# Kernel optimization log

Hardware: AMD Instinct MI355X
Metric: run time of the kernel (lower is better)

The kernel has to match this reference:

```python
import jax, jax.numpy as jnp
import numpy as np

EMBED_DIM = 1024
NUM_HEADS = 16
HEAD_DIM = EMBED_DIM // NUM_HEADS
B, S = 2, 2048


def setup_inputs() -> dict:
    key = jax.random.key(0)
    ks = jax.random.split(key, 12)
    sd = 1.0 / np.sqrt(EMBED_DIM)
    def lin(kw, kb):
        W = jax.random.uniform(kw, (EMBED_DIM, EMBED_DIM), jnp.float32, -sd, sd)
        b = jax.random.uniform(kb, (EMBED_DIM,), jnp.float32, -sd, sd)
        return W, b
    Wq, bq = lin(ks[0], ks[1])
    Wk, bk = lin(ks[2], ks[3])
    Wv, bv = lin(ks[4], ks[5])
    Wo, bo = lin(ks[6], ks[7])
    q = jax.random.normal(ks[8], (B, S, EMBED_DIM), jnp.float32)
    k = jax.random.normal(ks[9], (B, S, EMBED_DIM), jnp.float32)
    v = jax.random.normal(ks[10], (B, S, EMBED_DIM), jnp.float32)
    # broadcastable causal mask: True = keep (mask==0 positions get -inf)
    attn_mask = jnp.tril(jnp.ones((S, S), jnp.bool_))[None, None]
    return {"q": q, "k": k, "v": v,
            "Wq": Wq, "bq": bq, "Wk": Wk, "bk": bk,
            "Wv": Wv, "bv": bv, "Wo": Wo, "bo": bo,
            "attn_mask": attn_mask}


def reference(q, k, v, Wq, bq, Wk, bk, Wv, bv, Wo, bo, attn_mask):
    bsz, tgt_len, _ = q.shape
    src_len = k.shape[1]
    scale = jnp.sqrt(jnp.float32(HEAD_DIM))
    # projections: PyTorch Linear is x @ W.T + b
    qh = (q @ Wq.T + bq).reshape(bsz, tgt_len, NUM_HEADS, HEAD_DIM).transpose(0, 2, 1, 3)
    kh = (k @ Wk.T + bk).reshape(bsz, src_len, NUM_HEADS, HEAD_DIM).transpose(0, 2, 1, 3)
    vh = (v @ Wv.T + bv).reshape(bsz, src_len, NUM_HEADS, HEAD_DIM).transpose(0, 2, 1, 3)
    # [B,H,T,S] scores
    scores = jnp.einsum('bhtd,bhsd->bhts', qh, kh) / scale
    scores = jnp.where(attn_mask, scores, -jnp.inf)
    attn = jax.nn.softmax(scores, axis=-1)
    out = jnp.einsum('bhts,bhsd->bhtd', attn, vh)  # [B,H,T,D]
    out = out.transpose(0, 2, 1, 3).reshape(bsz, tgt_len, EMBED_DIM)
    return out @ Wo.T + bo
```

## Files before the change

### kernel.cpp

```cpp
#include <hip/hip_runtime.h>
#include <hip/hip_bf16.h>
#include <stdint.h>
#include <stddef.h>

typedef __hip_bfloat16 bf16_t;
typedef __attribute__((ext_vector_type(8))) short short8;
typedef __attribute__((ext_vector_type(4))) short short4v;
typedef __attribute__((ext_vector_type(4))) float floatx4;

#define EMBED 1024
#define NHEAD 16
#define HDIM  64
#define BATCH 2
#define SEQ   2048
#define MTOT  (BATCH*SEQ)
#define NEG_INF (-1e30f)
#define SCALE2 0.18033688011112042f

#define MFMA16(a,b,c) __builtin_amdgcn_mfma_f32_16x16x32_bf16(a,b,c,0,0,0)

static __device__ __forceinline__ short bf16_bits(float x) {
    return __builtin_bit_cast(short, __float2bfloat16(x));
}

static __device__ __forceinline__ float fast_exp2(float x) {
#if __has_builtin(__builtin_amdgcn_exp2f)
    return __builtin_amdgcn_exp2f(x);
#else
    return __expf(x * 0.6931471805599453f);
#endif
}

static __device__ __forceinline__ void async_ld16(const bf16_t* g, short* l) {
    __builtin_amdgcn_global_load_lds(
        (const __attribute__((address_space(1))) void*)g,
        (__attribute__((address_space(3))) void*)l,
        16, 0, 0);
}

static __device__ __forceinline__ void store_out(float* p, float v)  { *p = v; }
static __device__ __forceinline__ void store_out(bf16_t* p, float v) { *p = __float2bfloat16(v); }

__global__ __launch_bounds__(256)
void cvt_all(const float* __restrict__ q, const float* __restrict__ k, const float* __restrict__ v,
             const float* __restrict__ wq, const float* __restrict__ wk,
             const float* __restrict__ wv, const float* __restrict__ wo,
             bf16_t* __restrict__ Qx, bf16_t* __restrict__ Kx, bf16_t* __restrict__ Vx,
             bf16_t* __restrict__ Wqb, bf16_t* __restrict__ Wkb,
             bf16_t* __restrict__ Wvb, bf16_t* __restrict__ Wob)
{
    const float* s; bf16_t* d; int n;
    switch (blockIdx.y) {
        case 0:  s = q;  d = Qx;  n = MTOT * EMBED;  break;
        case 1:  s = k;  d = Kx;  n = MTOT * EMBED;  break;
        case 2:  s = v;  d = Vx;  n = MTOT * EMBED;  break;
        case 3:  s = wq; d = Wqb; n = EMBED * EMBED; break;
        case 4:  s = wk; d = Wkb; n = EMBED * EMBED; break;
        case 5:  s = wv; d = Wvb; n = EMBED * EMBED; break;
        default: s = wo; d = Wob; n = EMBED * EMBED; break;
    }
    const int i4 = (int)blockIdx.x * 256 + (int)threadIdx.x;
    if (i4 * 4 < n) {
        const float4 f = ((const float4*)s)[i4];
        short4v o;
        o[0] = bf16_bits(f.x); o[1] = bf16_bits(f.y);
        o[2] = bf16_bits(f.z); o[3] = bf16_bits(f.w);
        ((short4v*)d)[i4] = o;
    }
}

template <typename OutT, bool VT>
static __device__ __forceinline__ void gemm_tile_128(
    const bf16_t* __restrict__ A, const bf16_t* __restrict__ W,
    const float* __restrict__ bias, OutT* __restrict__ C)
{
    const int N = 1024, K = 1024;
    __shared__ alignas(16) short As[128*32];
    __shared__ alignas(16) short Bs[128*32];

    const int tid  = threadIdx.x;
    const int wave = tid >> 6;
    const int lane = tid & 63;
    const int nbn = N >> 7;
    const int bm = (int)blockIdx.x / nbn;
    const int bn = (int)blockIdx.x % nbn;
    const int m0 = bm << 7, n0 = bn << 7;

    const int wm = ((wave >> 1) & 1) << 6;
    const int wn = (wave & 1) << 6;

    floatx4 acc[4][4] = {};

    const int srow = (wave << 5) + (lane >> 2);
    const int scol = (lane & 3) << 3;
    const bf16_t* gA = A + (size_t)(m0 + srow) * K + scol;
    const bf16_t* gB = W + (size_t)(n0 + srow) * K + scol;
    short* lA0 = &As[(wave << 10)];
    short* lA1 = &As[(wave << 10) + 512];
    short* lB0 = &Bs[(wave << 10)];
    short* lB1 = &Bs[(wave << 10) + 512];

    const int fr = lane & 15;
    const int fk = (lane >> 4) << 3;

    for (int k0 = 0; k0 < K; k0 += 32) {
        __syncthreads();
        async_ld16(gA,                  lA0);
        async_ld16(gA + (size_t)16 * K, lA1);
        async_ld16(gB,                  lB0);
        async_ld16(gB + (size_t)16 * K, lB1);
        gA += 32; gB += 32;
        __syncthreads();

        short8 af[4], bfr[4];
        #pragma unroll
        for (int i = 0; i < 4; ++i)
            af[i] = *(const short8*)&As[(wm + (i << 4) + fr) * 32 + fk];
        #pragma unroll
        for (int j = 0; j < 4; ++j)
            bfr[j] = *(const short8*)&Bs[(wn + (j << 4) + fr) * 32 + fk];
        #pragma unroll
        for (int i = 0; i < 4; ++i)
            #pragma unroll
            for (int j = 0; j < 4; ++j)
                acc[i][j] = MFMA16(af[i], bfr[j], acc[i][j]);
    }

    const int q4 = (lane >> 4) << 2;
    #pragma unroll
    for (int j = 0; j < 4; ++j) {
        const int n = n0 + wn + (j << 4) + fr;
        const float bv = bias[n];
        #pragma unroll
        for (int i = 0; i < 4; ++i) {
            const int mb = m0 + wm + (i << 4) + q4;
            if (VT) {
                const int bb = mb >> 11, ss = mb & 2047;
                short4v pk;
                #pragma unroll
                for (int r = 0; r < 4; ++r)
                    pk[r] = bf16_bits(acc[i][j][r] + bv);
                *(short4v*)((bf16_t*)C + ((size_t)(bb * 1024 + n) << 11) + ss) = pk;
            } else {
                #pragma unroll
                for (int r = 0; r < 4; ++r)
                    store_out(&C[(size_t)(mb + r) * N + n], acc[i][j][r] + bv);
            }
        }
    }
}

__global__ __launch_bounds__(256)
void qkv_proj(const bf16_t* __restrict__ xq, const bf16_t* __restrict__ xk,
              const bf16_t* __restrict__ xv,
              const bf16_t* __restrict__ Wq, const bf16_t* __restrict__ Wk,
              const bf16_t* __restrict__ Wv,
              const float* __restrict__ bq, const float* __restrict__ bk,
              const float* __restrict__ bv,
              bf16_t* __restrict__ Qp, bf16_t* __restrict__ Kp, bf16_t* __restrict__ Vtp)
{
    if (blockIdx.z == 0)      gemm_tile_128<bf16_t, false>(xq, Wq, bq, Qp);
    else if (blockIdx.z == 1) gemm_tile_128<bf16_t, false>(xk, Wk, bk, Kp);
    else                      gemm_tile_128<bf16_t, true >(xv, Wv, bv, Vtp);
}

__global__ __launch_bounds__(256)
void out_proj(const bf16_t* __restrict__ AO, const bf16_t* __restrict__ Wo,
              const float* __restrict__ bo, float* __restrict__ out)
{
    gemm_tile_128<float, false>(AO, Wo, bo, out);
}

__global__ __launch_bounds__(64)
void attn_causal(const bf16_t* __restrict__ Qp, const bf16_t* __restrict__ Kp,
                 const bf16_t* __restrict__ Vt, bf16_t* __restrict__ AO)
{
    __shared__ alignas(16) short Pbuf[2][16 * 40];

    const int lane = (int)threadIdx.x & 63;
    const int bid  = (int)blockIdx.x;
    const int bh   = bid & 31;
    const int tile = 63 - (bid >> 5);
    const int b = bh >> 4, h = bh & 15;
    const int q0  = tile << 5;
    const int nch = tile + 1;

    const int fr   = lane & 15;
    const int quad = lane >> 4;
    const int fk   = quad << 3;

    const bf16_t* Q0 = Qp + (size_t)(b * SEQ + q0 + fr) * EMBED + h * HDIM;
    const short8 aq00 = *(const short8*)(Q0 + fk);
    const short8 aq01 = *(const short8*)(Q0 + 32 + fk);
    const short8 aq10 = *(const short8*)(Q0 + (size_t)16 * EMBED + fk);
    const short8 aq11 = *(const short8*)(Q0 + (size_t)16 * EMBED + 32 + fk);

    const bf16_t* Kbase = Kp + (size_t)(b * SEQ) * EMBED + h * HDIM;
    const bf16_t* Vbase = Vt + ((size_t)(b * 1024 + h * HDIM) << 11);

    floatx4 o0[4] = {}, o1[4] = {};
    float m0 = NEG_INF, m1 = NEG_INF;
    float l0 = 0.f, l1 = 0.f;

    short* Pw0 = &Pbuf[0][0];
    short* Pw1 = &Pbuf[1][0];

    auto smax = [&](const floatx4& sA, const floatx4& sB, float& m_u, float& l_u,
                    floatx4* o_u, short* PwU, const bool diag, const int u16) -> short8 {
        float v0[4], v1[4];
        float mx = NEG_INF;
        #pragma unroll
        for (int r = 0; r < 4; ++r) {
            float a  = sA[r] * SCALE2;
            float bb = sB[r] * SCALE2;
            if (diag) {
                const int kq = (quad << 2) + r;
                const int lq = u16 + fr;
                if (kq > lq)      a  = NEG_INF;
                if (kq + 16 > lq) bb = NEG_INF;
            }
            v0[r] = a; v1[r] = bb;
            mx = fmaxf(mx, fmaxf(a, bb));
        }
        mx = fmaxf(mx, __shfl_xor(mx, 16, 64));
        mx = fmaxf(mx, __shfl_xor(mx, 32, 64));
        const float mo = m_u;
        const bool need = __any(mx > mo + 8.0f) != 0;
        const float mn = need ? fmaxf(mo, mx) : mo;
        float ls = 0.f;
        #pragma unroll
        for (int r = 0; r < 4; ++r) {
            v0[r] = fast_exp2(v0[r] - mn);
            v1[r] = fast_exp2(v1[r] - mn);
            ls += v0[r] + v1[r];
        }
        ls += __shfl_xor(ls, 16, 64);
        ls += __shfl_xor(ls, 32, 64);
        if (need) {
            const float al = fast_exp2(mo - mn);
            m_u = mn;
            l_u = l_u * al + ls;
            #pragma unroll
            for (int r = 0; r < 4; ++r) {
                const float ao = __shfl(al, (lane & 48) | ((quad << 2) + r), 64);
                #pragma unroll
                for (int t = 0; t < 4; ++t) o_u[t][r] *= ao;
            }
        } else {
            l_u += ls;
        }
        short4v w0, w1;
        #pragma unroll
        for (int r = 0; r < 4; ++r) { w0[r] = bf16_bits(v0[r]); w1[r] = bf16_bits(v1[r]); }
        *(short4v*)&PwU[fr * 40 + (quad << 2)]      = w0;
        *(short4v*)&PwU[fr * 40 + 16 + (quad << 2)] = w1;
        __asm__ volatile("" ::: "memory");
        const short8 pa = *(const short8*)&PwU[fr * 40 + fk];
        __asm__ volatile("" ::: "memory");
        return pa;
    };

#define KLOAD(K0_, K1_, K2_, K3_, kvo) do {                                  \
        const bf16_t* Kr0_ = Kbase + (size_t)((kvo) + fr) * EMBED;           \
        const bf16_t* Kr1_ = Kr0_ + (size_t)16 * EMBED;                      \
        K0_ = *(const short8*)(Kr0_ + fk);                                   \
        K1_ = *(const short8*)(Kr0_ + 32 + fk);                              \
        K2_ = *(const short8*)(Kr1_ + fk);                                   \
        K3_ = *(const short8*)(Kr1_ + 32 + fk);                              \
    } while (0)

#define ITER(KC0, KC1, KC2, KC3, KN0, KN1, KN2, KN3, DIAGF) do {             \
        const int kv0 = c << 5;                                              \
           \
        const short8 vf0 = *(const short8*)(Vbase + ((size_t)(fr)      << 11) + kv0 + fk); \
        const short8 vf1 = *(const short8*)(Vbase + ((size_t)(16 + fr) << 11) + kv0 + fk); \
        const short8 vf2 = *(const short8*)(Vbase + ((size_t)(32 + fr) << 11) + kv0 + fk); \
        const short8 vf3 = *(const short8*)(Vbase + ((size_t)(48 + fr) << 11) + kv0 + fk); \
        floatx4 s00 = {}, s01 = {}, s10 = {}, s11 = {};                      \
        s00 = MFMA16(KC0, aq00, s00); s00 = MFMA16(KC1, aq01, s00);          \
        s10 = MFMA16(KC0, aq10, s10); s10 = MFMA16(KC1, aq11, s10);          \
        s01 = MFMA16(KC2, aq00, s01); s01 = MFMA16(KC3, aq01, s01);          \
        s11 = MFMA16(KC2, aq10, s11); s11 = MFMA16(KC3, aq11, s11);          \
        if (c + 1 < nch) { KLOAD(KN0, KN1, KN2, KN3, kv0 + 32); }            \
        const short8 pa0 = smax(s00, s01, m0, l0, o0, Pw0, DIAGF, 0);        \
        const short8 pa1 = smax(s10, s11, m1, l1, o1, Pw1, DIAGF, 16);       \
        o0[0] = MFMA16(pa0, vf0, o0[0]); o1[0] = MFMA16(pa1, vf0, o1[0]);    \
        o0[1] = MFMA16(pa0, vf1, o0[1]); o1[1] = MFMA16(pa1, vf1, o1[1]);    \
        o0[2] = MFMA16(pa0, vf2, o0[2]); o1[2] = MFMA16(pa1, vf2, o1[2]);    \
        o0[3] = MFMA16(pa0, vf3, o0[3]); o1[3] = MFMA16(pa1, vf3, o1[3]);    \
    } while (0)

    short8 ka0, ka1, ka2, ka3, kb0, kb1, kb2, kb3;
    KLOAD(ka0, ka1, ka2, ka3, 0);

    int c = 0;
    if (nch > 1) {
        for (;;) {
            ITER(ka0, ka1, ka2, ka3, kb0, kb1, kb2, kb3, false);
            if (++c == nch - 1) break;
            ITER(kb0, kb1, kb2, kb3, ka0, ka1, ka2, ka3, false);
            if (++c == nch - 1) break;
        }
    }
    if (c & 1) { ITER(kb0, kb1, kb2, kb3, ka0, ka1, ka2, ka3, true); }
    else       { ITER(ka0, ka1, ka2, ka3, kb0, kb1, kb2, kb3, true); }

#undef ITER
#undef KLOAD

    const float r0 = 1.0f / l0;
    const float r1 = 1.0f / l1;
    #pragma unroll
    for (int r = 0; r < 4; ++r) {
        const int src = (lane & 48) | ((quad << 2) + r);
        const float i0 = __shfl(r0, src, 64);
        const float i1 = __shfl(r1, src, 64);
        const int row0 = q0 + (quad << 2) + r;
        bf16_t* out0 = AO + (size_t)(b * SEQ + row0) * EMBED + h * HDIM + fr;
        bf16_t* out1 = out0 + (size_t)16 * EMBED;
        #pragma unroll
        for (int t = 0; t < 4; ++t) {
            out0[t << 4] = __float2bfloat16(o0[t][r] * i0);
            out1[t << 4] = __float2bfloat16(o1[t][r] * i1);
        }
    }
}

extern "C" void kernel_launch(void* const* d_in, const int* in_sizes, int n_in,
                              void* d_out, int out_size, void* d_ws, size_t ws_size,
                              hipStream_t stream)
{
    (void)in_sizes; (void)n_in; (void)out_size; (void)ws_size;
    const float* q  = (const float*)d_in[0];
    const float* k  = (const float*)d_in[1];
    const float* v  = (const float*)d_in[2];
    const float* Wq = (const float*)d_in[3];
    const float* bq = (const float*)d_in[4];
    const float* Wk = (const float*)d_in[5];
    const float* bk = (const float*)d_in[6];
    const float* Wv = (const float*)d_in[7];
    const float* bv = (const float*)d_in[8];
    const float* Wo = (const float*)d_in[9];
    const float* bo = (const float*)d_in[10];

    const size_t NX = (size_t)MTOT * EMBED;
    const size_t NW = (size_t)EMBED * EMBED;
    bf16_t* Qx  = (bf16_t*)d_ws;
    bf16_t* Kx  = Qx  + NX;
    bf16_t* Vx  = Kx  + NX;
    bf16_t* Wqb = Vx  + NX;
    bf16_t* Wkb = Wqb + NW;
    bf16_t* Wvb = Wkb + NW;
    bf16_t* Wob = Wvb + NW;
    bf16_t* Qp  = Wob + NW;
    bf16_t* Kp  = Qp  + NX;
    bf16_t* Vtp = Kp  + NX;
    bf16_t* AO  = Vtp + NX;

    dim3 blk(256);
    cvt_all<<<dim3(4096, 7), blk, 0, stream>>>(q, k, v, Wq, Wk, Wv, Wo,
                                               Qx, Kx, Vx, Wqb, Wkb, Wvb, Wob);
    qkv_proj<<<dim3(256, 1, 3), blk, 0, stream>>>(Qx, Kx, Vx, Wqb, Wkb, Wvb,
                                                  bq, bk, bv, Qp, Kp, Vtp);
    attn_causal<<<dim3(2048), dim3(64), 0, stream>>>(Qp, Kp, Vtp, AO);
    out_proj<<<dim3(256), blk, 0, stream>>>(AO, Wob, bo, (float*)d_out);
}
```

Measured before the change: 284.8 us.

## Split long causal attention tiles across two blocks and merge partials

The 32 longest query tiles per head are split into two halves of the key range, each run by its own block, which writes unnormalized fp32 partial outputs plus row max and row sum to workspace. A new combine kernel then merges the two halves with log-sum-exp weighting. The goal is to balance the causal triangle and shorten the critical path of the attention kernel. The softmax is also reworked to skip the cross-lane max and sum reductions unless a rescale is needed, deferring the row-sum reduction to the end. This costs an extra kernel launch and the workspace traffic for the partials.

```diff
diff --git a/kernel.cpp b/kernel.cpp
--- a/kernel.cpp
+++ b/kernel.cpp
@@ -173,17 +173,35 @@
 
 __global__ __launch_bounds__(64)
 void attn_causal(const bf16_t* __restrict__ Qp, const bf16_t* __restrict__ Kp,
-                 const bf16_t* __restrict__ Vt, bf16_t* __restrict__ AO)
+                 const bf16_t* __restrict__ Vt, bf16_t* __restrict__ AO,
+                 float* __restrict__ Op, float* __restrict__ Mp, float* __restrict__ Lp)
 {
     __shared__ alignas(16) short Pbuf[2][16 * 40];
 
     const int lane = (int)threadIdx.x & 63;
     const int bid  = (int)blockIdx.x;
     const int bh   = bid & 31;
-    const int tile = 63 - (bid >> 5);
+    const int w    = bid >> 5;
+    int tile, sidx, c0, c1;
+    bool split;
+    if (w < 64) {
+        tile  = 63 - (w >> 1);
+        sidx  = w & 1;
+        split = true;
+        const int nch = tile + 1;
+        const int h1  = (nch + 1) >> 1;
+        c0 = sidx ? h1 : 0;
+        c1 = sidx ? nch : h1;
+    } else {
+        tile  = 95 - w;
+        sidx  = 0;
+        split = false;
+        c0 = 0;
+        c1 = tile + 1;
+    }
+    const bool hasdiag = (c1 == tile + 1);
     const int b = bh >> 4, h = bh & 15;
-    const int q0  = tile << 5;
-    const int nch = tile + 1;
+    const int q0 = tile << 5;
 
     const int fr   = lane & 15;
     const int quad = lane >> 4;
@@ -205,9 +223,9 @@
     short* Pw0 = &Pbuf[0][0];
     short* Pw1 = &Pbuf[1][0];
 
-    auto smax = [&](const floatx4& sA, const floatx4& sB, float& m_u, float& l_u,
-                    floatx4* o_u, short* PwU, const bool diag, const int u16) -> short8 {
-        float v0[4], v1[4];
+    auto smax_vals = [&](const floatx4& sA, const floatx4& sB, float& m_u, float& l_u,
+                         floatx4* o_u, const bool diag, const int u16,
+                         float* v0, float* v1) {
         float mx = NEG_INF;
         #pragma unroll
         for (int r = 0; r < 4; ++r) {
@@ -222,42 +240,28 @@
             v0[r] = a; v1[r] = bb;
             mx = fmaxf(mx, fmaxf(a, bb));
         }
-        mx = fmaxf(mx, __shfl_xor(mx, 16, 64));
-        mx = fmaxf(mx, __shfl_xor(mx, 32, 64));
-        const float mo = m_u;
-        const bool need = __any(mx > mo + 8.0f) != 0;
-        const float mn = need ? fmaxf(mo, mx) : mo;
-        float ls = 0.f;
-        #pragma unroll
-        for (int r = 0; r < 4; ++r) {
-            v0[r] = fast_exp2(v0[r] - mn);
-            v1[r] = fast_exp2(v1[r] - mn);
-            ls += v0[r] + v1[r];
-        }
-        ls += __shfl_xor(ls, 16, 64);
-        ls += __shfl_xor(ls, 32, 64);
-        if (need) {
-            const float al = fast_exp2(mo - mn);
+        if (__any(mx > m_u + 8.0f)) {
+            mx = fmaxf(mx, __shfl_xor(mx, 16, 64));
+            mx = fmaxf(mx, __shfl_xor(mx, 32, 64));
+            const float mn = fmaxf(m_u, mx);
+            const float al = fast_exp2(m_u - mn);
             m_u = mn;
-            l_u = l_u * al + ls;
+            l_u *= al;
             #pragma unroll
             for (int r = 0; r < 4; ++r) {
                 const float ao = __shfl(al, (lane & 48) | ((quad << 2) + r), 64);
                 #pragma unroll
                 for (int t = 0; t < 4; ++t) o_u[t][r] *= ao;
             }
-        } else {
-            l_u += ls;
-        }
-        short4v w0, w1;
-        #pragma unroll
-        for (int r = 0; r < 4; ++r) { w0[r] = bf16_bits(v0[r]); w1[r] = bf16_bits(v1[r]); }
-        *(short4v*)&PwU[fr * 40 + (quad << 2)]      = w0;
-        *(short4v*)&PwU[fr * 40 + 16 + (quad << 2)] = w1;
-        __asm__ volatile("" ::: "memory");
-        const short8 pa = *(const short8*)&PwU[fr * 40 + fk];
-        __asm__ volatile("" ::: "memory");
-        return pa;
+        }
+        float ls = 0.f;
+        #pragma unroll
+        for (int r = 0; r < 4; ++r) {
+            v0[r] = fast_exp2(v0[r] - m_u);
+            v1[r] = fast_exp2(v1[r] - m_u);
+            ls += v0[r] + v1[r];
+        }
+        l_u += ls;
     };
 
 #define KLOAD(K0_, K1_, K2_, K3_, kvo) do {                                  \
@@ -269,7 +273,7 @@
         K3_ = *(const short8*)(Kr1_ + 32 + fk);                              \
     } while (0)
 
-#define ITER(KC0, KC1, KC2, KC3, KN0, KN1, KN2, KN3, DIAGF) do {             \
+#define ITER(KC0, KC1, KC2, KC3, KN0, KN1, KN2, KN3, DIAGF, PREF) do {       \
         const int kv0 = c << 5;                                              \
            \
         const short8 vf0 = *(const short8*)(Vbase + ((size_t)(fr)      << 11) + kv0 + fk); \
@@ -281,9 +285,24 @@
         s10 = MFMA16(KC0, aq10, s10); s10 = MFMA16(KC1, aq11, s10);          \
         s01 = MFMA16(KC2, aq00, s01); s01 = MFMA16(KC3, aq01, s01);          \
         s11 = MFMA16(KC2, aq10, s11); s11 = MFMA16(KC3, aq11, s11);          \
-        if (c + 1 < nch) { KLOAD(KN0, KN1, KN2, KN3, kv0 + 32); }            \
-        const short8 pa0 = smax(s00, s01, m0, l0, o0, Pw0, DIAGF, 0);        \
-        const short8 pa1 = smax(s10, s11, m1, l1, o1, Pw1, DIAGF, 16);       \
+        if (PREF) { KLOAD(KN0, KN1, KN2, KN3, kv0 + 32); }                   \
+        float p00[4], p01[4], p10[4], p11[4];                                \
+        smax_vals(s00, s01, m0, l0, o0, DIAGF, 0,  p00, p01);                \
+        smax_vals(s10, s11, m1, l1, o1, DIAGF, 16, p10, p11);                \
+        short4v wa0, wa1, wb0, wb1;                                          \
+        _Pragma("unroll")                                                    \
+        for (int r = 0; r < 4; ++r) {                                        \
+            wa0[r] = bf16_bits(p00[r]); wa1[r] = bf16_bits(p01[r]);          \
+            wb0[r] = bf16_bits(p10[r]); wb1[r] = bf16_bits(p11[r]);          \
+        }                                                                    \
+        *(short4v*)&Pw0[fr * 40 + (quad << 2)]      = wa0;                   \
+        *(short4v*)&Pw0[fr * 40 + 16 + (quad << 2)] = wa1;                   \
+        *(short4v*)&Pw1[fr * 40 + (quad << 2)]      = wb0;                   \
+        *(short4v*)&Pw1[fr * 40 + 16 + (quad << 2)] = wb1;                   \
+        __asm__ volatile("" ::: "memory");     \
+        const short8 pa0 = *(const short8*)&Pw0[fr * 40 + fk];               \
+        const short8 pa1 = *(const short8*)&Pw1[fr * 40 + fk];               \
+        __asm__ volatile("" ::: "memory");                                   \
         o0[0] = MFMA16(pa0, vf0, o0[0]); o1[0] = MFMA16(pa1, vf0, o1[0]);    \
         o0[1] = MFMA16(pa0, vf1, o0[1]); o1[1] = MFMA16(pa1, vf1, o1[1]);    \
         o0[2] = MFMA16(pa0, vf2, o0[2]); o1[2] = MFMA16(pa1, vf2, o1[2]);    \
@@ -291,39 +310,103 @@
     } while (0)
 
     short8 ka0, ka1, ka2, ka3, kb0, kb1, kb2, kb3;
-    KLOAD(ka0, ka1, ka2, ka3, 0);
-
-    int c = 0;
-    if (nch > 1) {
+    KLOAD(ka0, ka1, ka2, ka3, c0 << 5);
+
+    int c = c0;
+    const int cl = c1 - 1;
+    if (cl > c0) {
         for (;;) {
-            ITER(ka0, ka1, ka2, ka3, kb0, kb1, kb2, kb3, false);
-            if (++c == nch - 1) break;
-            ITER(kb0, kb1, kb2, kb3, ka0, ka1, ka2, ka3, false);
-            if (++c == nch - 1) break;
-        }
-    }
-    if (c & 1) { ITER(kb0, kb1, kb2, kb3, ka0, ka1, ka2, ka3, true); }
-    else       { ITER(ka0, ka1, ka2, ka3, kb0, kb1, kb2, kb3, true); }
+            ITER(ka0, ka1, ka2, ka3, kb0, kb1, kb2, kb3, false, true);
+            if (++c == cl) break;
+            ITER(kb0, kb1, kb2, kb3, ka0, ka1, ka2, ka3, false, true);
+            if (++c == cl) break;
+        }
+    }
+    if ((c - c0) & 1) { ITER(kb0, kb1, kb2, kb3, ka0, ka1, ka2, ka3, hasdiag, false); }
+    else              { ITER(ka0, ka1, ka2, ka3, kb0, kb1, kb2, kb3, hasdiag, false); }
 
 #undef ITER
 #undef KLOAD
 
-    const float r0 = 1.0f / l0;
-    const float r1 = 1.0f / l1;
-    #pragma unroll
-    for (int r = 0; r < 4; ++r) {
-        const int src = (lane & 48) | ((quad << 2) + r);
-        const float i0 = __shfl(r0, src, 64);
-        const float i1 = __shfl(r1, src, 64);
-        const int row0 = q0 + (quad << 2) + r;
-        bf16_t* out0 = AO + (size_t)(b * SEQ + row0) * EMBED + h * HDIM + fr;
-        bf16_t* out1 = out0 + (size_t)16 * EMBED;
-        #pragma unroll
-        for (int t = 0; t < 4; ++t) {
-            out0[t << 4] = __float2bfloat16(o0[t][r] * i0);
-            out1[t << 4] = __float2bfloat16(o1[t][r] * i1);
-        }
-    }
+    { float t = __shfl_xor(l0, 16, 64); l0 += t; t = __shfl_xor(l0, 32, 64); l0 += t; }
+    { float t = __shfl_xor(l1, 16, 64); l1 += t; t = __shfl_xor(l1, 32, 64); l1 += t; }
+
+    if (!split) {
+        const float r0 = 1.0f / l0;
+        const float r1 = 1.0f / l1;
+        #pragma unroll
+        for (int r = 0; r < 4; ++r) {
+            const int src = (lane & 48) | ((quad << 2) + r);
+            const float i0 = __shfl(r0, src, 64);
+            const float i1 = __shfl(r1, src, 64);
+            const int row0 = q0 + (quad << 2) + r;
+            bf16_t* out0 = AO + (size_t)(b * SEQ + row0) * EMBED + h * HDIM + fr;
+            bf16_t* out1 = out0 + (size_t)16 * EMBED;
+            #pragma unroll
+            for (int t = 0; t < 4; ++t) {
+                out0[t << 4] = __float2bfloat16(o0[t][r] * i0);
+                out1[t << 4] = __float2bfloat16(o1[t][r] * i1);
+            }
+        }
+    } else {
+        const int p = (bh << 5) | (tile - 32);
+        float* Ob = Op + (((size_t)sidx << 10) + p) * 2048;
+        #pragma unroll
+        for (int r = 0; r < 4; ++r) {
+            const int row0 = (quad << 2) + r;
+            #pragma unroll
+            for (int t = 0; t < 4; ++t) {
+                Ob[row0 * 64 + (t << 4) + fr]        = o0[t][r];
+                Ob[(16 + row0) * 64 + (t << 4) + fr] = o1[t][r];
+            }
+        }
+        if (quad == 0) {
+            const size_t mb = (((size_t)sidx << 10) + p) * 32;
+            Mp[mb + fr]      = m0;
+            Mp[mb + 16 + fr] = m1;
+            Lp[mb + fr]      = l0;
+            Lp[mb + 16 + fr] = l1;
+        }
+    }
+}
+
+__global__ __launch_bounds__(256)
+void attn_combine(const float* __restrict__ Op, const float* __restrict__ Mp,
+                  const float* __restrict__ Lp, bf16_t* __restrict__ AO)
+{
+    const int p   = (int)blockIdx.x;
+    const int tid = (int)threadIdx.x;
+    const int row = tid >> 3;
+    const int d0  = (tid & 7) << 3;
+    const int bh = p >> 5, tile = 32 + (p & 31);
+    const int b = bh >> 4, h = bh & 15;
+
+    const float m0 = Mp[(size_t)p * 32 + row];
+    const float m1 = Mp[(size_t)(1024 + p) * 32 + row];
+    const float l0 = Lp[(size_t)p * 32 + row];
+    const float l1 = Lp[(size_t)(1024 + p) * 32 + row];
+    const float M  = fmaxf(m0, m1);
+    const float w0 = fast_exp2(m0 - M);
+    const float w1 = fast_exp2(m1 - M);
+    const float rd = 1.0f / (l0 * w0 + l1 * w1);
+
+    const float* O0 = Op + ((size_t)p << 11) + row * 64 + d0;
+    const float* O1 = O0 + ((size_t)1024 << 11);
+    const float4 a0 = *(const float4*)O0;
+    const float4 a1 = *(const float4*)(O0 + 4);
+    const float4 c0 = *(const float4*)O1;
+    const float4 c1 = *(const float4*)(O1 + 4);
+
+    short8 pk;
+    pk[0] = bf16_bits((a0.x * w0 + c0.x * w1) * rd);
+    pk[1] = bf16_bits((a0.y * w0 + c0.y * w1) * rd);
+    pk[2] = bf16_bits((a0.z * w0 + c0.z * w1) * rd);
+    pk[3] = bf16_bits((a0.w * w0 + c0.w * w1) * rd);
+    pk[4] = bf16_bits((a1.x * w0 + c1.x * w1) * rd);
+    pk[5] = bf16_bits((a1.y * w0 + c1.y * w1) * rd);
+    pk[6] = bf16_bits((a1.z * w0 + c1.z * w1) * rd);
+    pk[7] = bf16_bits((a1.w * w0 + c1.w * w1) * rd);
+    *(short8*)(AO + (size_t)(b * SEQ + tile * 32 + row) * EMBED + h * HDIM + d0) = pk;
 }
 
 extern "C" void kernel_launch(void* const* d_in, const int* in_sizes, int n_in,
@@ -357,11 +440,16 @@
     bf16_t* Vtp = Kp  + NX;
     bf16_t* AO  = Vtp + NX;
 
+    float* Op = (float*)Qx;
+    float* Mp = (float*)Wqb;
+    float* Lp = Mp + 2 * 1024 * 32;
+
     dim3 blk(256);
     cvt_all<<<dim3(4096, 7), blk, 0, stream>>>(q, k, v, Wq, Wk, Wv, Wo,
                                                Qx, Kx, Vx, Wqb, Wkb, Wvb, Wob);
     qkv_proj<<<dim3(256, 1, 3), blk, 0, stream>>>(Qx, Kx, Vx, Wqb, Wkb, Wvb,
                                                   bq, bk, bv, Qp, Kp, Vtp);
-    attn_causal<<<dim3(2048), dim3(64), 0, stream>>>(Qp, Kp, Vtp, AO);
+    attn_causal<<<dim3(3072), dim3(64), 0, stream>>>(Qp, Kp, Vtp, AO, Op, Mp, Lp);
+    attn_combine<<<dim3(1024), blk, 0, stream>>>(Op, Mp, Lp, AO);
     out_proj<<<dim3(256), blk, 0, stream>>>(AO, Wob, bo, (float*)d_out);
 }
```

Result: no change. 286.7 us (+0.7%).
